# Optimization experiments

Measured on AMD Instinct MI355X. Metric: run time of the kernel, lower is better.

Reference implementation:

```python
import math
import jax, jax.numpy as jnp
import numpy as np

B, T, C = 2, 2048, 1024
N_HEAD = 16
HEAD_DIM = C // N_HEAD


def setup_inputs() -> dict:
    key = jax.random.key(0)
    k1, k2, k3 = jax.random.split(key, 3)
    x = jax.random.normal(k1, (B, T, C), dtype=jnp.float32)
    w_attn = jax.random.normal(k2, (3 * C, C), dtype=jnp.float32) * 0.02
    w_proj = jax.random.normal(k3, (C, C), dtype=jnp.float32) * 0.02
    return {"x": x, "w_attn": w_attn, "w_proj": w_proj}


def _rope_cos_sin(seq_len, dim, dtype):
    inv_freq = 1.0 / (10000.0 ** (jnp.arange(0, dim, 2, dtype=jnp.float32) / dim))
    t = jnp.arange(seq_len, dtype=jnp.float32)
    freqs = jnp.einsum('i,j->ij', t, inv_freq)          # [T, dim/2]
    emb = jnp.concatenate([freqs, freqs], axis=-1)       # [T, dim]
    return jnp.cos(emb).astype(dtype), jnp.sin(emb).astype(dtype)


def _rotate_half(x):
    x1, x2 = jnp.split(x, 2, axis=-1)
    return jnp.concatenate([-x2, x1], axis=-1)


def _apply_rope(x, cos, sin):
    # x: [B, H, T, D]; cos/sin: [T, D] broadcast over batch/head
    return x * cos[None, None] + _rotate_half(x) * sin[None, None]


def reference(x, w_attn, w_proj):
    b, t, c = x.shape
    h, d = N_HEAD, c // N_HEAD
    qkv = x @ w_attn.T                                   # [B, T, 3C]
    q, k, v = jnp.split(qkv, 3, axis=-1)
    q = q.reshape(b, t, h, d).transpose(0, 2, 1, 3)      # [B, H, T, D]
    k = k.reshape(b, t, h, d).transpose(0, 2, 1, 3)
    v = v.reshape(b, t, h, d).transpose(0, 2, 1, 3)
    cos, sin = _rope_cos_sin(t, d, x.dtype)
    q = _apply_rope(q, cos, sin)
    k = _apply_rope(k, cos, sin)
    logits = jnp.einsum('bhqd,bhkd->bhqk', q, k) * (1.0 / math.sqrt(d))
    causal = jnp.tril(jnp.ones((t, t), dtype=bool))
    logits = jnp.where(causal[None, None], logits, jnp.float32(-jnp.inf).astype(logits.dtype))
    att = jax.nn.softmax(logits, axis=-1)                # [B, H, T, T]
    y = jnp.einsum('bhqk,bhkd->bhqd', att, v)            # [B, H, T, D]
    y = y.transpose(0, 2, 1, 3).reshape(b, t, c)
    return y @ w_proj.T
```

## Files before the change

kernel.cpp:

```cpp
#include <hip/hip_runtime.h>
#include <hip/hip_bf16.h>
#include <math.h>

#define B_ 2
#define T_ 2048
#define C_ 1024
#define H_ 16

typedef __bf16 bf16x8 __attribute__((ext_vector_type(8)));
typedef __bf16 bf16x4 __attribute__((ext_vector_type(4)));
typedef float f32x4 __attribute__((ext_vector_type(4)));
typedef float f32x16 __attribute__((ext_vector_type(16)));
typedef unsigned int u32;

#if __has_builtin(__builtin_amdgcn_exp2f)
#define EXP2(x) __builtin_amdgcn_exp2f(x)
#else
#define EXP2(x) exp2f(x)
#endif

__device__ __forceinline__ void gload16(const void* g, void* l) {
    __builtin_amdgcn_global_load_lds(
        (const __attribute__((address_space(1))) void*)g,
        (__attribute__((address_space(3))) void*)l, 16, 0, 0);
}

__device__ __forceinline__ f32x4 mfma16(bf16x8 a, bf16x8 b, f32x4 c) {
    return __builtin_amdgcn_mfma_f32_16x16x32_bf16(a, b, c, 0, 0, 0);
}
__device__ __forceinline__ f32x16 mfma32(bf16x8 a, bf16x8 b, f32x16 c) {
    return __builtin_amdgcn_mfma_f32_32x32x16_bf16(a, b, c, 0, 0, 0);
}

__device__ __forceinline__ u32 cvtpk(float lo, float hi) {
    u32 r;
    asm("v_cvt_pk_bf16_f32 %0, %1, %2" : "=v"(r) : "v"(lo), "v"(hi));
    return r;
}

__device__ __forceinline__ void plane32swap(u32& a, u32& b) {
#if __has_builtin(__builtin_amdgcn_permlane32_swap)
    auto r = __builtin_amdgcn_permlane32_swap(a, b, false, false);
    a = r[0]; b = r[1];
#else
    asm("v_permlane32_swap_b32 %0, %1" : "+v"(a), "+v"(b));
#endif
}

#define SCLQ 0.18033688011112042f
#define NLOG2_10K_32 (-0.4152410118609203f)

__global__ __launch_bounds__(256) void cast_all(const float* __restrict__ x,
                                                const float* __restrict__ wa,
                                                const float* __restrict__ wp,
                                                __bf16* __restrict__ xb,
                                                __bf16* __restrict__ wab,
                                                __bf16* __restrict__ wpb) {
    const int i = blockIdx.x * 256 + threadIdx.x;
    const float* src;
    __bf16* dst;
    int k;
    if (i < 1048576)               { src = x;  dst = xb;  k = i; }
    else if (i < 1048576 + 786432) { src = wa; dst = wab; k = i - 1048576; }
    else                           { src = wp; dst = wpb; k = i - (1048576 + 786432); }
    float4 v = ((const float4*)src)[k];
    bf16x4 o;
    o[0] = (__bf16)v.x; o[1] = (__bf16)v.y; o[2] = (__bf16)v.z; o[3] = (__bf16)v.w;
    ((bf16x4*)dst)[k] = o;
}

__global__ __launch_bounds__(256) void gemm_qkv(const __bf16* __restrict__ A,
                                                const __bf16* __restrict__ Bw,
                                                __bf16* __restrict__ Qb,
                                                __bf16* __restrict__ Kb,
                                                __bf16* __restrict__ Vt) {
    const int tid  = threadIdx.x;
    const int lane = tid & 63;
    const int w    = tid >> 6;
    const int wr = w >> 1, wc = w & 1;
    const int l15 = lane & 15, lg = lane >> 4;
    const int bm = blockIdx.y * 128, bn = blockIdx.x * 128;
    const int K = C_;
    __shared__ __bf16 Asm[128 * 64];
    __shared__ __bf16 Bsm[128 * 64];
    f32x4 acc[4][4] = {};

    for (int kt = 0; kt < K; kt += 64) {
        if (kt) __syncthreads();
#pragma unroll
        for (int it = 0; it < 4; ++it) {
            const int c = it * 256 + tid;
            const int row = c >> 3, cc = (c & 7) * 8;
            gload16(A  + (size_t)(bm + row) * K + kt + cc, Asm + c * 8);
            gload16(Bw + (size_t)(bn + row) * K + kt + cc, Bsm + c * 8);
        }
        __syncthreads();
#pragma unroll
        for (int kk = 0; kk < 64; kk += 32) {
            bf16x8 af[4], bf[4];
#pragma unroll
            for (int i = 0; i < 4; ++i)
                af[i] = *(const bf16x8*)&Asm[(wr * 64 + i * 16 + l15) * 64 + kk + lg * 8];
#pragma unroll
            for (int j = 0; j < 4; ++j)
                bf[j] = *(const bf16x8*)&Bsm[(wc * 64 + j * 16 + l15) * 64 + kk + lg * 8];
#pragma unroll
            for (int i = 0; i < 4; ++i)
#pragma unroll
                for (int j = 0; j < 4; ++j)
                    acc[i][j] = mfma16(af[i], bf[j], acc[i][j]);
        }
    }
    const int region  = bn >> 10;
    const int colbase = (bn & 1023) + wc * 64;
    const int h = colbase >> 6;
    if (region < 2) {
        __bf16* dst = region ? Kb : Qb;
        const float scl = region ? 1.0f : SCLQ;
#pragma unroll
        for (int j = 0; j < 2; ++j) {
            const int d = j * 16 + l15;
            const float invf = exp2f((float)d * NLOG2_10K_32);
#pragma unroll
            for (int i = 0; i < 4; ++i)
#pragma unroll
                for (int r = 0; r < 4; ++r) {
                    const int row = bm + wr * 64 + i * 16 + lg * 4 + r;
                    const int b = row >> 11, t = row & (T_ - 1);
                    float sv, cv;
                    __sincosf((float)t * invf, &sv, &cv);
                    const float v1 = acc[i][j][r], v2 = acc[i][j + 2][r];
                    const float o1 = (v1 * cv - v2 * sv) * scl;
                    const float o2 = (v2 * cv + v1 * sv) * scl;
                    const size_t base = ((size_t)(b * H_ + h) * T_ + t) * 64;
                    dst[base + d]      = (__bf16)o1;
                    dst[base + d + 32] = (__bf16)o2;
                }
        }
    } else {
#pragma unroll
        for (int i = 0; i < 4; ++i)
#pragma unroll
            for (int j = 0; j < 4; ++j) {
                const int vcol = colbase + j * 16 + l15;
                const int hh = vcol >> 6, d = vcol & 63;
                const int row0 = bm + wr * 64 + i * 16 + lg * 4;
                const int b = row0 >> 11, t0 = row0 & (T_ - 1);
                u32 dw[2];
                dw[0] = cvtpk(acc[i][j][0], acc[i][j][1]);
                dw[1] = cvtpk(acc[i][j][2], acc[i][j][3]);
                *(uint64_t*)&Vt[((size_t)(b * H_ + hh) * 64 + d) * T_ + t0] =
                    *(uint64_t*)dw;
            }
    }
}

__global__ __launch_bounds__(256) void gemm_proj(const __bf16* __restrict__ A,
                                                 const __bf16* __restrict__ Bw,
                                                 float* __restrict__ Cp,
                                                 int N, int K) {
    const int tid  = threadIdx.x;
    const int lane = tid & 63;
    const int w    = tid >> 6;
    const int wr = w >> 1, wc = w & 1;
    const int l15 = lane & 15, lg = lane >> 4;
    const int bm = blockIdx.y * 64, bn = blockIdx.x * 128;
    __shared__ __bf16 Asm[64 * 64];
    __shared__ __bf16 Bsm[128 * 64];
    f32x4 acc[2][4] = {};

    for (int kt = 0; kt < K; kt += 64) {
        if (kt) __syncthreads();
#pragma unroll
        for (int it = 0; it < 2; ++it) {
            const int g = it * 256 + tid;
            const int row = g >> 3, cc = (g & 7) * 8;
            gload16(A + (size_t)(bm + row) * K + kt + cc, Asm + g * 8);
        }
#pragma unroll
        for (int it = 0; it < 4; ++it) {
            const int g = it * 256 + tid;
            const int row = g >> 3, cc = (g & 7) * 8;
            gload16(Bw + (size_t)(bn + row) * K + kt + cc, Bsm + g * 8);
        }
        __syncthreads();
#pragma unroll
        for (int kk = 0; kk < 64; kk += 32) {
            bf16x8 af[2], bf[4];
#pragma unroll
            for (int i = 0; i < 2; ++i)
                af[i] = *(const bf16x8*)&Asm[(wr * 32 + i * 16 + l15) * 64 + kk + lg * 8];
#pragma unroll
            for (int j = 0; j < 4; ++j)
                bf[j] = *(const bf16x8*)&Bsm[(wc * 64 + j * 16 + l15) * 64 + kk + lg * 8];
#pragma unroll
            for (int i = 0; i < 2; ++i)
#pragma unroll
                for (int j = 0; j < 4; ++j)
                    acc[i][j] = mfma16(af[i], bf[j], acc[i][j]);
        }
    }
#pragma unroll
    for (int i = 0; i < 2; ++i)
#pragma unroll
        for (int j = 0; j < 4; ++j)
#pragma unroll
            for (int r = 0; r < 4; ++r) {
                const int row = bm + wr * 32 + i * 16 + lg * 4 + r;
                const int col = bn + wc * 64 + j * 16 + l15;
                Cp[(size_t)row * N + col] = acc[i][j][r];
            }
}

__global__ __launch_bounds__(256) void attn_fwd(const __bf16* __restrict__ Qb,
                                                const __bf16* __restrict__ Kb,
                                                const __bf16* __restrict__ Vt,
                                                __bf16* __restrict__ Yatt) {
    const int gid = blockIdx.x;
    const int bh = (gid & 7) * 4 + ((gid >> 3) & 3);
    const int qq = gid >> 5;
    const int qt = (qq < 8) ? (15 - qq) : (qq - 8);
    const int b = bh >> 4, h = bh & 15;
    const int tid = threadIdx.x, lane = tid & 63, w = tid >> 6;
    const int l31 = lane & 31, hi = lane >> 5;
    const int hi4 = hi * 4;
    __shared__ __bf16 Ksm[2][128 * 64];
    __shared__ __bf16 Vsm[2][64 * 128];

    const int Q0 = qt * 128 + w * 32;
    const int qg = Q0 + l31;
    const __bf16* Qp = Qb + ((size_t)bh * T_ + Q0) * 64;
    const __bf16* Kp = Kb + (size_t)bh * T_ * 64;
    const __bf16* Vp = Vt + (size_t)bh * 64 * T_;

    auto STAGE = [&](int j) {
        __bf16* Ks = Ksm[j & 1];
        __bf16* Vs = Vsm[j & 1];
#pragma unroll
        for (int it = 0; it < 4; ++it) {
            const int g = it * 256 + tid;
            const int kr = g >> 3, kc = (g & 7) ^ (kr & 7);
            gload16(Kp + ((size_t)(j * 128 + kr)) * 64 + kc * 8, Ks + g * 8);
            const int vd = g >> 4, vg = (g & 15) ^ (vd & 15);
            gload16(Vp + (size_t)vd * T_ + j * 128 + vg * 8, Vs + g * 8);
        }
    };

    const int jmax = qt + 1;
    STAGE(0);

    bf16x8 qf[4];
#pragma unroll
    for (int ds = 0; ds < 4; ++ds)
        qf[ds] = *(const bf16x8*)&Qp[l31 * 64 + ds * 16 + hi * 8];

    f32x16 ot[2] = {};
    float l_run = 0.f;

    for (int j = 0; j < jmax; ++j) {
        const int cur = j & 1;
        __builtin_amdgcn_s_barrier();
        if (j + 1 < jmax) {
            STAGE(j + 1);
            asm volatile("s_waitcnt vmcnt(8)" ::: "memory");
        } else {
            asm volatile("s_waitcnt vmcnt(0)" ::: "memory");
        }
        __builtin_amdgcn_s_barrier();
        __builtin_amdgcn_sched_barrier(0);

        f32x16 st[4] = {};
#pragma unroll
        for (int a = 0; a < 4; ++a)
#pragma unroll
            for (int ds = 0; ds < 4; ++ds) {
                const int row = a * 32 + l31;
                const int off = (ds * 32 + hi * 16) ^ ((row & 7) << 4);
                bf16x8 kf = *(const bf16x8*)((const char*)Ksm[cur] + row * 128 + off);
                st[a] = mfma32(kf, qf[ds], st[a]);
            }
        if (j == qt) {
#pragma unroll
            for (int a = 0; a < 4; ++a)
#pragma unroll
                for (int r = 0; r < 16; ++r) {
                    const int kv = j * 128 + a * 32 + (r & 3) + 8 * (r >> 2) + hi4;
                    if (kv > qg) st[a][r] = -1e30f;
                }
        }
        float s0 = 0.f, s1 = 0.f;
#pragma unroll
        for (int a = 0; a < 4; ++a)
#pragma unroll
            for (int r = 0; r < 16; ++r) {
                const float e = EXP2(st[a][r]);
                st[a][r] = e;
                if (r & 1) s1 += e; else s0 += e;
            }
        float rs = s0 + s1;
        rs += __shfl_xor(rs, 32);
        l_run += rs;
        bf16x8 pa[8];
#pragma unroll
        for (int ks = 0; ks < 8; ++ks) {
            const int a = ks >> 1, rb = (ks & 1) * 8;
            u32 X0 = cvtpk(st[a][rb + 0], st[a][rb + 1]);
            u32 X1 = cvtpk(st[a][rb + 2], st[a][rb + 3]);
            u32 Y0 = cvtpk(st[a][rb + 4], st[a][rb + 5]);
            u32 Y1 = cvtpk(st[a][rb + 6], st[a][rb + 7]);
            plane32swap(X0, Y0);
            plane32swap(X1, Y1);
            u32 dw[4] = {X0, X1, Y0, Y1};
            pa[ks] = *(bf16x8*)dw;
        }
#pragma unroll
        for (int ks = 0; ks < 8; ++ks)
#pragma unroll
            for (int db = 0; db < 2; ++db) {
                const int row = db * 32 + l31;
                const int off = ((ks * 2 + hi) ^ (row & 15)) * 16;
                bf16x8 vf = *(const bf16x8*)((const char*)Vsm[cur] + row * 256 + off);
                ot[db] = mfma32(vf, pa[ks], ot[db]);
            }
    }
    const float inv = 1.f / l_run;
    __bf16* Yp = Yatt + ((size_t)(b * T_ + qg)) * C_ + h * 64;
#pragma unroll
    for (int db = 0; db < 2; ++db)
#pragma unroll
        for (int rq = 0; rq < 4; ++rq) {
            const int r = rq * 4;
            u32 dw[2];
            dw[0] = cvtpk(ot[db][r] * inv,     ot[db][r + 1] * inv);
            dw[1] = cvtpk(ot[db][r + 2] * inv, ot[db][r + 3] * inv);
            const int d = db * 32 + 8 * rq + hi4;
            *(uint64_t*)&Yp[d] = *(uint64_t*)dw;
        }
}

extern "C" void kernel_launch(void* const* d_in, const int* in_sizes, int n_in,
                              void* d_out, int out_size, void* d_ws, size_t ws_size,
                              hipStream_t stream) {
    const float* x      = (const float*)d_in[0];
    const float* w_attn = (const float*)d_in[1];
    const float* w_proj = (const float*)d_in[2];
    float* out = (float*)d_out;
    char* ws = (char*)d_ws;

    __bf16* xb  = (__bf16*)(ws);
    __bf16* wab = (__bf16*)(ws + 8388608);
    __bf16* wpb = (__bf16*)(ws + 14680064);
    __bf16* Qb  = (__bf16*)(ws + 16777216);
    __bf16* Kb  = (__bf16*)(ws + 25165824);
    __bf16* Vt  = (__bf16*)(ws + 33554432);
    __bf16* Ya  = (__bf16*)(ws + 41943040);

    cast_all<<<dim3(8192), 256, 0, stream>>>(x, w_attn, w_proj, xb, wab, wpb);

    gemm_qkv<<<dim3(3 * C_ / 128, B_ * T_ / 128), 256, 0, stream>>>(
        xb, wab, Qb, Kb, Vt);

    attn_fwd<<<dim3(16 * 32), 256, 0, stream>>>(Qb, Kb, Vt, Ya);

    gemm_proj<<<dim3(C_ / 128, B_ * T_ / 64), 256, 0, stream>>>(
        Ya, wpb, out, C_, C_);
}
```

Baseline: 105.0 us.

## Split attention KV tile across two wave groups with LDS reduction

Doubles the attention block to 512 threads. Each group of four waves handles half of every 128-key tile for the same query rows, and waves skip key halves that lie fully above the causal diagonal. At the end the partial outputs and row sums are combined through shared memory. The goal is more waves per CU for latency hiding and less wasted compute on masked tiles, at the cost of an extra barrier and LDS reduction step and more register pressure from the launch-bounds constraint. Softmax has no running max, so adding the partial sums directly is valid.

```diff
diff --git a/kernel.cpp b/kernel.cpp
--- a/kernel.cpp
+++ b/kernel.cpp
@@ -212,22 +212,23 @@
             }
 }
 
-__global__ __launch_bounds__(256) void attn_fwd(const __bf16* __restrict__ Qb,
-                                                const __bf16* __restrict__ Kb,
-                                                const __bf16* __restrict__ Vt,
-                                                __bf16* __restrict__ Yatt) {
+__global__ __launch_bounds__(512, 4) void attn_fwd(const __bf16* __restrict__ Qb,
+                                                   const __bf16* __restrict__ Kb,
+                                                   const __bf16* __restrict__ Vt,
+                                                   __bf16* __restrict__ Yatt) {
     const int gid = blockIdx.x;
     const int bh = (gid & 7) * 4 + ((gid >> 3) & 3);
     const int qq = gid >> 5;
     const int qt = (qq < 8) ? (15 - qq) : (qq - 8);
     const int b = bh >> 4, h = bh & 15;
     const int tid = threadIdx.x, lane = tid & 63, w = tid >> 6;
+    const int qgrp = w & 3, kvh = w >> 2;
     const int l31 = lane & 31, hi = lane >> 5;
     const int hi4 = hi * 4;
     __shared__ __bf16 Ksm[2][128 * 64];
     __shared__ __bf16 Vsm[2][64 * 128];
 
-    const int Q0 = qt * 128 + w * 32;
+    const int Q0 = qt * 128 + qgrp * 32;
     const int qg = Q0 + l31;
     const __bf16* Qp = Qb + ((size_t)bh * T_ + Q0) * 64;
     const __bf16* Kp = Kb + (size_t)bh * T_ * 64;
@@ -237,8 +238,8 @@
         __bf16* Ks = Ksm[j & 1];
         __bf16* Vs = Vsm[j & 1];
 #pragma unroll
-        for (int it = 0; it < 4; ++it) {
-            const int g = it * 256 + tid;
+        for (int it = 0; it < 2; ++it) {
+            const int g = it * 512 + tid;
             const int kr = g >> 3, kc = (g & 7) ^ (kr & 7);
             gload16(Kp + ((size_t)(j * 128 + kr)) * 64 + kc * 8, Ks + g * 8);
             const int vd = g >> 4, vg = (g & 15) ^ (vd & 15);
@@ -262,80 +263,113 @@
         __builtin_amdgcn_s_barrier();
         if (j + 1 < jmax) {
             STAGE(j + 1);
-            asm volatile("s_waitcnt vmcnt(8)" ::: "memory");
+            asm volatile("s_waitcnt vmcnt(4)" ::: "memory");
         } else {
             asm volatile("s_waitcnt vmcnt(0)" ::: "memory");
         }
         __builtin_amdgcn_s_barrier();
         __builtin_amdgcn_sched_barrier(0);
 
-        f32x16 st[4] = {};
-#pragma unroll
-        for (int a = 0; a < 4; ++a)
-#pragma unroll
-            for (int ds = 0; ds < 4; ++ds) {
-                const int row = a * 32 + l31;
-                const int off = (ds * 32 + hi * 16) ^ ((row & 7) << 4);
-                bf16x8 kf = *(const bf16x8*)((const char*)Ksm[cur] + row * 128 + off);
-                st[a] = mfma32(kf, qf[ds], st[a]);
-            }
-        if (j == qt) {
-#pragma unroll
-            for (int a = 0; a < 4; ++a)
+        if (j * 128 + kvh * 64 <= Q0 + 31) {
+            f32x16 st[2] = {};
+#pragma unroll
+            for (int a = 0; a < 2; ++a)
+#pragma unroll
+                for (int ds = 0; ds < 4; ++ds) {
+                    const int row = kvh * 64 + a * 32 + l31;
+                    const int off = (ds * 32 + hi * 16) ^ ((row & 7) << 4);
+                    bf16x8 kf = *(const bf16x8*)((const char*)Ksm[cur] + row * 128 + off);
+                    st[a] = mfma32(kf, qf[ds], st[a]);
+                }
+            if (j == qt) {
+#pragma unroll
+                for (int a = 0; a < 2; ++a)
+#pragma unroll
+                    for (int r = 0; r < 16; ++r) {
+                        const int kv = j * 128 + kvh * 64 + a * 32 +
+                                       (r & 3) + 8 * (r >> 2) + hi4;
+                        if (kv > qg) st[a][r] = -1e30f;
+                    }
+            }
+            float s0 = 0.f, s1 = 0.f;
+#pragma unroll
+            for (int a = 0; a < 2; ++a)
 #pragma unroll
                 for (int r = 0; r < 16; ++r) {
-                    const int kv = j * 128 + a * 32 + (r & 3) + 8 * (r >> 2) + hi4;
-                    if (kv > qg) st[a][r] = -1e30f;
+                    const float e = EXP2(st[a][r]);
+                    st[a][r] = e;
+                    if (r & 1) s1 += e; else s0 += e;
                 }
-        }
-        float s0 = 0.f, s1 = 0.f;
-#pragma unroll
-        for (int a = 0; a < 4; ++a)
-#pragma unroll
-            for (int r = 0; r < 16; ++r) {
-                const float e = EXP2(st[a][r]);
-                st[a][r] = e;
-                if (r & 1) s1 += e; else s0 += e;
-            }
-        float rs = s0 + s1;
-        rs += __shfl_xor(rs, 32);
-        l_run += rs;
-        bf16x8 pa[8];
-#pragma unroll
-        for (int ks = 0; ks < 8; ++ks) {
-            const int a = ks >> 1, rb = (ks & 1) * 8;
-            u32 X0 = cvtpk(st[a][rb + 0], st[a][rb + 1]);
-            u32 X1 = cvtpk(st[a][rb + 2], st[a][rb + 3]);
-            u32 Y0 = cvtpk(st[a][rb + 4], st[a][rb + 5]);
-            u32 Y1 = cvtpk(st[a][rb + 6], st[a][rb + 7]);
-            plane32swap(X0, Y0);
-            plane32swap(X1, Y1);
-            u32 dw[4] = {X0, X1, Y0, Y1};
-            pa[ks] = *(bf16x8*)dw;
-        }
-#pragma unroll
-        for (int ks = 0; ks < 8; ++ks)
-#pragma unroll
-            for (int db = 0; db < 2; ++db) {
-                const int row = db * 32 + l31;
-                const int off = ((ks * 2 + hi) ^ (row & 15)) * 16;
-                bf16x8 vf = *(const bf16x8*)((const char*)Vsm[cur] + row * 256 + off);
-                ot[db] = mfma32(vf, pa[ks], ot[db]);
-            }
-    }
-    const float inv = 1.f / l_run;
-    __bf16* Yp = Yatt + ((size_t)(b * T_ + qg)) * C_ + h * 64;
-#pragma unroll
-    for (int db = 0; db < 2; ++db)
-#pragma unroll
-        for (int rq = 0; rq < 4; ++rq) {
-            const int r = rq * 4;
-            u32 dw[2];
-            dw[0] = cvtpk(ot[db][r] * inv,     ot[db][r + 1] * inv);
-            dw[1] = cvtpk(ot[db][r + 2] * inv, ot[db][r + 3] * inv);
-            const int d = db * 32 + 8 * rq + hi4;
-            *(uint64_t*)&Yp[d] = *(uint64_t*)dw;
-        }
+            float rs = s0 + s1;
+            rs += __shfl_xor(rs, 32);
+            l_run += rs;
+            bf16x8 pa[4];
+#pragma unroll
+            for (int ks = 0; ks < 4; ++ks) {
+                const int a = ks >> 1, rb = (ks & 1) * 8;
+                u32 X0 = cvtpk(st[a][rb + 0], st[a][rb + 1]);
+                u32 X1 = cvtpk(st[a][rb + 2], st[a][rb + 3]);
+                u32 Y0 = cvtpk(st[a][rb + 4], st[a][rb + 5]);
+                u32 Y1 = cvtpk(st[a][rb + 6], st[a][rb + 7]);
+                plane32swap(X0, Y0);
+                plane32swap(X1, Y1);
+                u32 dw[4] = {X0, X1, Y0, Y1};
+                pa[ks] = *(bf16x8*)dw;
+            }
+#pragma unroll
+            for (int ks = 0; ks < 4; ++ks)
+#pragma unroll
+                for (int db = 0; db < 2; ++db) {
+                    const int row = db * 32 + l31;
+                    const int gnl = (kvh * 8 + ks * 2 + hi) ^ (row & 15);
+                    bf16x8 vf = *(const bf16x8*)((const char*)Vsm[cur] +
+                                                 row * 256 + gnl * 16);
+                    ot[db] = mfma32(vf, pa[ks], ot[db]);
+                }
+        }
+    }
+    __builtin_amdgcn_s_barrier();
+    f32x4* m4 = (f32x4*)&Ksm[0][0];
+    float* lb = (float*)&Vsm[0][0];
+    if (w >= 4) {
+        const int woff = (w - 4) * 64 + lane;
+#pragma unroll
+        for (int db = 0; db < 2; ++db)
+#pragma unroll
+            for (int rq = 0; rq < 4; ++rq) {
+                f32x4 v;
+                v[0] = ot[db][rq * 4 + 0]; v[1] = ot[db][rq * 4 + 1];
+                v[2] = ot[db][rq * 4 + 2]; v[3] = ot[db][rq * 4 + 3];
+                m4[(db * 4 + rq) * 256 + woff] = v;
+            }
+        lb[woff] = l_run;
+    }
+    __builtin_amdgcn_s_barrier();
+    if (w < 4) {
+        const int woff = w * 64 + lane;
+#pragma unroll
+        for (int db = 0; db < 2; ++db)
+#pragma unroll
+            for (int rq = 0; rq < 4; ++rq) {
+                f32x4 v = m4[(db * 4 + rq) * 256 + woff];
+                ot[db][rq * 4 + 0] += v[0]; ot[db][rq * 4 + 1] += v[1];
+                ot[db][rq * 4 + 2] += v[2]; ot[db][rq * 4 + 3] += v[3];
+            }
+        l_run += lb[woff];
+        const float inv = 1.f / l_run;
+        __bf16* Yp = Yatt + ((size_t)(b * T_ + qg)) * C_ + h * 64;
+#pragma unroll
+        for (int db = 0; db < 2; ++db)
+#pragma unroll
+            for (int rq = 0; rq < 4; ++rq) {
+                const int r = rq * 4;
+                u32 dw[2];
+                dw[0] = cvtpk(ot[db][r] * inv,     ot[db][r + 1] * inv);
+                dw[1] = cvtpk(ot[db][r + 2] * inv, ot[db][r + 3] * inv);
+                const int d = db * 32 + 8 * rq + hi4;
+                *(uint64_t*)&Yp[d] = *(uint64_t*)dw;
+            }
+    }
 }
 
 extern "C" void kernel_launch(void* const* d_in, const int* in_sizes, int n_in,
@@ -360,7 +394,7 @@
     gemm_qkv<<<dim3(3 * C_ / 128, B_ * T_ / 128), 256, 0, stream>>>(
         xb, wab, Qb, Kb, Vt);
 
-    attn_fwd<<<dim3(16 * 32), 256, 0, stream>>>(Qb, Kb, Vt, Ya);
+    attn_fwd<<<dim3(16 * 32), 512, 0, stream>>>(Qb, Kb, Vt, Ya);
 
     gemm_proj<<<dim3(C_ / 128, B_ * T_ / 64), 256, 0, stream>>>(
         Ya, wpb, out, C_, C_);
```

Measured after the change: 100.5 us. 1.04x faster.
